# Kernel optimization log

Hardware: AMD Instinct MI355X
Metric: run time of the kernel (lower is better)

## Reference

```python
import jax, jax.numpy as jnp
import numpy as np

BATCH = 32      # init batch_size
HID = 256       # init hidden_dim
SENT = 64       # sentence_size
WORDS = 64      # words per sentence (the -1 in the view)
N = BATCH * SENT


def setup_inputs() -> dict:
    key = jax.random.key(0)
    k1, k2, k3, k4 = jax.random.split(key, 4)
    stdv_lin = 1.0 / np.sqrt(HID)
    x = jax.random.normal(k1, (N, WORDS, HID), dtype=jnp.float32)
    W = jax.random.uniform(k2, (HID, HID), jnp.float32, -stdv_lin, stdv_lin)
    b = jax.random.uniform(k3, (HID,), jnp.float32, -stdv_lin, stdv_lin)
    context = jax.random.uniform(k4, (HID,), jnp.float32, -stdv_lin, stdv_lin)
    return {"x": x, "W": W, "b": b, "context": context, "sentence_size": SENT}


def reference(x, W, b, context, sentence_size):
    # tanh(Linear(x)) applied per position; vectorized over the batch loop
    attends = jnp.tanh(jnp.einsum("nwh,oh->nwo", x, W) + b)  # [N, WORDS, HID]
    scores = attends * context                                 # [N, WORDS, HID]
    # nn.Softmax on the [-1, HID] view -> softmax over the hidden dim
    alpha = jax.nn.softmax(scores, axis=-1)                    # [N, WORDS, HID]
    attended = x * alpha                                       # legacy same-numel mul
    attended = attended.reshape(BATCH, sentence_size, -1, HID)
    return jnp.sum(attended, axis=2)                           # [BATCH, SENT, HID]
```

## Files before the change

kernel.cpp:

```cpp
#include <hip/hip_runtime.h>
#include <hip/hip_bf16.h>

#define HID 256
#define NROWS 2048
#define NITER 8
#define GRID (NROWS / NITER)
#define PITCH 264

typedef __attribute__((ext_vector_type(8))) short short8;
typedef __attribute__((ext_vector_type(4))) float float4v;
typedef __attribute__((ext_vector_type(4))) unsigned short ushort4v;

__device__ __forceinline__ float bf2f(unsigned short u) {
    return __uint_as_float(((unsigned int)u) << 16);
}

__device__ __forceinline__ unsigned int pk_bf16(float a, float b) {
    __hip_bfloat162 p = __float22bfloat162_rn(float2{a, b});
    return *(unsigned int*)&p;
}

__device__ __forceinline__ float tanh_fast(float x) {
    float e = __builtin_amdgcn_exp2f(x * 2.8853900817779268f);
    return 1.0f - 2.0f * __builtin_amdgcn_rcpf(e + 1.0f);
}

__device__ __forceinline__ float exp_small(float s) {
    float p = __builtin_fmaf(s, 0.16666667f, 0.5f);
    p = __builtin_fmaf(p, s, 1.0f);
    return __builtin_fmaf(p, s, 1.0f);
}

__device__ __forceinline__ void barrier_lds_only() {
    __asm__ volatile("" ::: "memory");
    __builtin_amdgcn_s_waitcnt(0xC07F);
    __builtin_amdgcn_s_barrier();
    __asm__ volatile("" ::: "memory");
}

__device__ __forceinline__ float row16_sum(float v) {
    float t;
    t = __builtin_bit_cast(float, __builtin_amdgcn_update_dpp(
            0, __builtin_bit_cast(int, v), 0xB1, 0xf, 0xf, true));
    v += t;
    t = __builtin_bit_cast(float, __builtin_amdgcn_update_dpp(
            0, __builtin_bit_cast(int, v), 0x4E, 0xf, 0xf, true));
    v += t;
    t = __builtin_bit_cast(float, __builtin_amdgcn_update_dpp(
            0, __builtin_bit_cast(int, v), 0x124, 0xf, 0xf, true));
    v += t;
    t = __builtin_bit_cast(float, __builtin_amdgcn_update_dpp(
            0, __builtin_bit_cast(int, v), 0x128, 0xf, 0xf, true));
    v += t;
    return v;
}

__global__ void cvt_w(const float* __restrict__ W, unsigned short* __restrict__ Wb) {
    int i = blockIdx.x * 256 + threadIdx.x;
    float4v v = ((const float4v*)W)[i];
    unsigned int lo = pk_bf16(v.x, v.y), hi = pk_bf16(v.z, v.w);
    ushort4v u;
    u.x = (unsigned short)lo; u.y = (unsigned short)(lo >> 16);
    u.z = (unsigned short)hi; u.w = (unsigned short)(hi >> 16);
    ((ushort4v*)Wb)[i] = u;
}

__global__ __launch_bounds__(512, 2) void attend_fused(
    const float* __restrict__ x, const unsigned short* __restrict__ Wb,
    const float* __restrict__ bias, const float* __restrict__ ctx,
    float* __restrict__ out)
{
    __shared__ unsigned short xs[2][64 * PITCH];
    __shared__ float wsum[8][64];
    __shared__ float rinv[64];

    const int tid  = threadIdx.x;
    const int wave = tid >> 6;
    const int lane = tid & 63;
    const int q    = lane >> 4;
    const int c    = lane & 15;
    const int obase = wave * 32;

    float bb[2], cc[2];
#pragma unroll
    for (int nt = 0; nt < 2; ++nt) {
        bb[nt] = bias[obase + 2 * c + nt];
        cc[nt] = ctx[obase + 2 * c + nt];
    }
    short8 bfrag[8][2];
#pragma unroll
    for (int nt = 0; nt < 2; ++nt) {
        const unsigned short* wr = &Wb[(size_t)(obase + 2 * c + nt) * 256 + q * 8];
#pragma unroll
        for (int kt = 0; kt < 8; ++kt)
            bfrag[kt][nt] = *(const short8*)(wr + kt * 32);
    }

    const int n0 = blockIdx.x * NITER;

    {
        const float4v* xg = (const float4v*)(x + (size_t)n0 * (64 * 256));
        float4v v0[8];
#pragma unroll
        for (int i = 0; i < 8; ++i)
            v0[i] = xg[tid + 512 * i];
#pragma unroll
        for (int i = 0; i < 8; ++i) {
            const int chunk = tid + 512 * i;
            const int r = chunk >> 6, col4 = (chunk & 63) * 4;
            uint2 u;
            u.x = pk_bf16(v0[i].x, v0[i].y);
            u.y = pk_bf16(v0[i].z, v0[i].w);
            *(uint2*)&xs[0][r * PITCH + col4] = u;
        }
    }
    __syncthreads();

    for (int it = 0; it < NITER; ++it) {
        const int n = n0 + it;
        const int cur = it & 1;

        float4v vbuf[8];
        if (it + 1 < NITER) {
            const float4v* xg = (const float4v*)(x + (size_t)(n + 1) * (64 * 256));
#pragma unroll
            for (int i = 0; i < 8; ++i)
                vbuf[i] = xg[tid + 512 * i];
        }

        float4v acc[4][2];
#pragma unroll
        for (int mt = 0; mt < 4; ++mt)
#pragma unroll
            for (int nt = 0; nt < 2; ++nt)
                acc[mt][nt] = (float4v){0.f, 0.f, 0.f, 0.f};

#pragma unroll
        for (int kt = 0; kt < 8; ++kt) {
            short8 a[4];
#pragma unroll
            for (int mt = 0; mt < 4; ++mt)
                a[mt] = *(const short8*)&xs[cur][(mt * 16 + c) * PITCH + kt * 32 + q * 8];
#pragma unroll
            for (int nt = 0; nt < 2; ++nt)
#pragma unroll
                for (int mt = 0; mt < 4; ++mt)
                    acc[mt][nt] = __builtin_amdgcn_mfma_f32_16x16x32_bf16(
                        a[mt], bfrag[kt][nt], acc[mt][nt], 0, 0, 0);
        }

        float psum[4][4];
#pragma unroll
        for (int mt = 0; mt < 4; ++mt)
#pragma unroll
            for (int r = 0; r < 4; ++r)
                psum[mt][r] = 0.f;

#pragma unroll
        for (int nt = 0; nt < 2; ++nt) {
#pragma unroll
            for (int mt = 0; mt < 4; ++mt) {
#pragma unroll
                for (int r = 0; r < 4; ++r) {
                    float s = tanh_fast(acc[mt][nt][r] + bb[nt]) * cc[nt];
                    float e = exp_small(s);
                    acc[mt][nt][r] = e;
                    psum[mt][r] += e;
                }
            }
        }
#pragma unroll
        for (int mt = 0; mt < 4; ++mt)
#pragma unroll
            for (int r = 0; r < 4; ++r)
                psum[mt][r] = row16_sum(psum[mt][r]);
        if (c == 0) {
#pragma unroll
            for (int mt = 0; mt < 4; ++mt)
#pragma unroll
                for (int r = 0; r < 4; ++r)
                    wsum[wave][mt * 16 + q * 4 + r] = psum[mt][r];
        }
        barrier_lds_only();
        if (tid < 64) {
            float t = wsum[0][tid] + wsum[1][tid] + wsum[2][tid] + wsum[3][tid]
                    + wsum[4][tid] + wsum[5][tid] + wsum[6][tid] + wsum[7][tid];
            rinv[tid] = __builtin_amdgcn_rcpf(t);
        }
        barrier_lds_only();

        float ri[4][4];
#pragma unroll
        for (int mt = 0; mt < 4; ++mt)
#pragma unroll
            for (int r = 0; r < 4; ++r)
                ri[mt][r] = rinv[mt * 16 + q * 4 + r];

        float outp[2] = {0.f, 0.f};
#pragma unroll
        for (int mt = 0; mt < 4; ++mt) {
#pragma unroll
            for (int r = 0; r < 4; ++r) {
                const int w = mt * 16 + q * 4 + r;
                unsigned int pair = *(const unsigned int*)&xs[cur][w * PITCH + obase + 2 * c];
                const float wgt = ri[mt][r];
                outp[0] += bf2f((unsigned short)pair)         * (acc[mt][0][r] * wgt);
                outp[1] += bf2f((unsigned short)(pair >> 16)) * (acc[mt][1][r] * wgt);
            }
        }
#pragma unroll
        for (int nt = 0; nt < 2; ++nt) {
            float v = outp[nt];
            v += __shfl_xor(v, 16);
            v += __shfl_xor(v, 32);
            outp[nt] = v;
        }
        if (q == 0)
            *(float2*)&out[(size_t)n * HID + obase + 2 * c] = float2{outp[0], outp[1]};

        if (it + 1 < NITER) {
#pragma unroll
            for (int i = 0; i < 8; ++i) {
                const int chunk = tid + 512 * i;
                const int r = chunk >> 6, col4 = (chunk & 63) * 4;
                uint2 u;
                u.x = pk_bf16(vbuf[i].x, vbuf[i].y);
                u.y = pk_bf16(vbuf[i].z, vbuf[i].w);
                *(uint2*)&xs[cur ^ 1][r * PITCH + col4] = u;
            }
            __syncthreads();
        }
    }
}

extern "C" void kernel_launch(void* const* d_in, const int* in_sizes, int n_in,
                              void* d_out, int out_size, void* d_ws, size_t ws_size,
                              hipStream_t stream) {
    const float* x    = (const float*)d_in[0];
    const float* W    = (const float*)d_in[1];
    const float* bias = (const float*)d_in[2];
    const float* ctx  = (const float*)d_in[3];
    unsigned short* Wb = (unsigned short*)d_ws;

    cvt_w<<<64, 256, 0, stream>>>(W, Wb);
    attend_fused<<<GRID, 512, 0, stream>>>(x, Wb, bias, ctx, (float*)d_out);
}
```

Baseline: 207.7 us.

## Use 256-thread blocks with 64 columns per wave and stream W fragments

Halves the block size to 4 waves, each computing 64 output columns instead of 32, and halves rows per block so the grid doubles. Instead of keeping all W bf16 fragments resident in registers, each k-step reloads W from global/L2 with a one-step-ahead prefetch, freeing registers for the larger accumulator tile and the 16-deep x prefetch buffer. The intent is more blocks and better latency hiding with fewer waves in the softmax reduction. The cost is repeated W loads from cache in every iteration and a larger per-thread x staging buffer.

Measured after the change: 265.6 us. 27.9% more time.

```diff
diff --git a/kernel.cpp b/kernel.cpp
--- a/kernel.cpp
+++ b/kernel.cpp
@@ -3,7 +3,7 @@
 
 #define HID 256
 #define NROWS 2048
-#define NITER 8
+#define NITER 4
 #define GRID (NROWS / NITER)
 #define PITCH 264
 
@@ -65,13 +65,13 @@
     ((ushort4v*)Wb)[i] = u;
 }
 
-__global__ __launch_bounds__(512, 2) void attend_fused(
+__global__ __launch_bounds__(256, 2) void attend_fused(
     const float* __restrict__ x, const unsigned short* __restrict__ Wb,
     const float* __restrict__ bias, const float* __restrict__ ctx,
     float* __restrict__ out)
 {
     __shared__ unsigned short xs[2][64 * PITCH];
-    __shared__ float wsum[8][64];
+    __shared__ float wsum[4][64];
     __shared__ float rinv[64];
 
     const int tid  = threadIdx.x;
@@ -79,34 +79,35 @@
     const int lane = tid & 63;
     const int q    = lane >> 4;
     const int c    = lane & 15;
-    const int obase = wave * 32;
-
-    float bb[2], cc[2];
-#pragma unroll
-    for (int nt = 0; nt < 2; ++nt) {
-        bb[nt] = bias[obase + 2 * c + nt];
-        cc[nt] = ctx[obase + 2 * c + nt];
+    const int obase = wave * 64;
+
+    int col[4];
+#pragma unroll
+    for (int nt = 0; nt < 4; ++nt)
+        col[nt] = obase + (nt >> 1) * 32 + 2 * c + (nt & 1);
+
+    float bb[4], cc[4];
+#pragma unroll
+    for (int nt = 0; nt < 4; ++nt) {
+        bb[nt] = bias[col[nt]];
+        cc[nt] = ctx[col[nt]];
     }
-    short8 bfrag[8][2];
-#pragma unroll
-    for (int nt = 0; nt < 2; ++nt) {
-        const unsigned short* wr = &Wb[(size_t)(obase + 2 * c + nt) * 256 + q * 8];
-#pragma unroll
-        for (int kt = 0; kt < 8; ++kt)
-            bfrag[kt][nt] = *(const short8*)(wr + kt * 32);
-    }
+    const unsigned short* wrow[4];
+#pragma unroll
+    for (int nt = 0; nt < 4; ++nt)
+        wrow[nt] = &Wb[(size_t)col[nt] * 256 + q * 8];
 
     const int n0 = blockIdx.x * NITER;
 
     {
         const float4v* xg = (const float4v*)(x + (size_t)n0 * (64 * 256));
-        float4v v0[8];
-#pragma unroll
-        for (int i = 0; i < 8; ++i)
-            v0[i] = xg[tid + 512 * i];
-#pragma unroll
-        for (int i = 0; i < 8; ++i) {
-            const int chunk = tid + 512 * i;
+        float4v v0[16];
+#pragma unroll
+        for (int i = 0; i < 16; ++i)
+            v0[i] = xg[tid + 256 * i];
+#pragma unroll
+        for (int i = 0; i < 16; ++i) {
+            const int chunk = tid + 256 * i;
             const int r = chunk >> 6, col4 = (chunk & 63) * 4;
             uint2 u;
             u.x = pk_bf16(v0[i].x, v0[i].y);
@@ -120,33 +121,46 @@
         const int n = n0 + it;
         const int cur = it & 1;
 
-        float4v vbuf[8];
+        float4v vbuf[16];
         if (it + 1 < NITER) {
             const float4v* xg = (const float4v*)(x + (size_t)(n + 1) * (64 * 256));
 #pragma unroll
-            for (int i = 0; i < 8; ++i)
-                vbuf[i] = xg[tid + 512 * i];
-        }
-
-        float4v acc[4][2];
-#pragma unroll
-        for (int mt = 0; mt < 4; ++mt)
-#pragma unroll
-            for (int nt = 0; nt < 2; ++nt)
+            for (int i = 0; i < 16; ++i)
+                vbuf[i] = xg[tid + 256 * i];
+        }
+
+        float4v acc[4][4];
+#pragma unroll
+        for (int mt = 0; mt < 4; ++mt)
+#pragma unroll
+            for (int nt = 0; nt < 4; ++nt)
                 acc[mt][nt] = (float4v){0.f, 0.f, 0.f, 0.f};
 
+        short8 bcur[4], bnxt[4];
+#pragma unroll
+        for (int nt = 0; nt < 4; ++nt)
+            bcur[nt] = *(const short8*)(wrow[nt]);
+
 #pragma unroll
         for (int kt = 0; kt < 8; ++kt) {
+            if (kt < 7) {
+#pragma unroll
+                for (int nt = 0; nt < 4; ++nt)
+                    bnxt[nt] = *(const short8*)(wrow[nt] + (kt + 1) * 32);
+            }
             short8 a[4];
 #pragma unroll
             for (int mt = 0; mt < 4; ++mt)
                 a[mt] = *(const short8*)&xs[cur][(mt * 16 + c) * PITCH + kt * 32 + q * 8];
 #pragma unroll
-            for (int nt = 0; nt < 2; ++nt)
+            for (int nt = 0; nt < 4; ++nt)
 #pragma unroll
                 for (int mt = 0; mt < 4; ++mt)
                     acc[mt][nt] = __builtin_amdgcn_mfma_f32_16x16x32_bf16(
-                        a[mt], bfrag[kt][nt], acc[mt][nt], 0, 0, 0);
+                        a[mt], bcur[nt], acc[mt][nt], 0, 0, 0);
+#pragma unroll
+            for (int nt = 0; nt < 4; ++nt)
+                bcur[nt] = bnxt[nt];
         }
 
         float psum[4][4];
@@ -157,7 +171,7 @@
                 psum[mt][r] = 0.f;
 
 #pragma unroll
-        for (int nt = 0; nt < 2; ++nt) {
+        for (int nt = 0; nt < 4; ++nt) {
 #pragma unroll
             for (int mt = 0; mt < 4; ++mt) {
 #pragma unroll
@@ -183,8 +197,7 @@
         }
         barrier_lds_only();
         if (tid < 64) {
-            float t = wsum[0][tid] + wsum[1][tid] + wsum[2][tid] + wsum[3][tid]
-                    + wsum[4][tid] + wsum[5][tid] + wsum[6][tid] + wsum[7][tid];
+            float t = wsum[0][tid] + wsum[1][tid] + wsum[2][tid] + wsum[3][tid];
             rinv[tid] = __builtin_amdgcn_rcpf(t);
         }
         barrier_lds_only();
@@ -196,32 +209,37 @@
             for (int r = 0; r < 4; ++r)
                 ri[mt][r] = rinv[mt * 16 + q * 4 + r];
 
-        float outp[2] = {0.f, 0.f};
+        float outp[4] = {0.f, 0.f, 0.f, 0.f};
 #pragma unroll
         for (int mt = 0; mt < 4; ++mt) {
 #pragma unroll
             for (int r = 0; r < 4; ++r) {
                 const int w = mt * 16 + q * 4 + r;
-                unsigned int pair = *(const unsigned int*)&xs[cur][w * PITCH + obase + 2 * c];
                 const float wgt = ri[mt][r];
-                outp[0] += bf2f((unsigned short)pair)         * (acc[mt][0][r] * wgt);
-                outp[1] += bf2f((unsigned short)(pair >> 16)) * (acc[mt][1][r] * wgt);
-            }
-        }
-#pragma unroll
-        for (int nt = 0; nt < 2; ++nt) {
+                unsigned int p0 = *(const unsigned int*)&xs[cur][w * PITCH + obase + 2 * c];
+                unsigned int p1 = *(const unsigned int*)&xs[cur][w * PITCH + obase + 32 + 2 * c];
+                outp[0] += bf2f((unsigned short)p0)         * (acc[mt][0][r] * wgt);
+                outp[1] += bf2f((unsigned short)(p0 >> 16)) * (acc[mt][1][r] * wgt);
+                outp[2] += bf2f((unsigned short)p1)         * (acc[mt][2][r] * wgt);
+                outp[3] += bf2f((unsigned short)(p1 >> 16)) * (acc[mt][3][r] * wgt);
+            }
+        }
+#pragma unroll
+        for (int nt = 0; nt < 4; ++nt) {
             float v = outp[nt];
             v += __shfl_xor(v, 16);
             v += __shfl_xor(v, 32);
             outp[nt] = v;
         }
-        if (q == 0)
-            *(float2*)&out[(size_t)n * HID + obase + 2 * c] = float2{outp[0], outp[1]};
+        if (q == 0) {
+            *(float2*)&out[(size_t)n * HID + obase + 2 * c]      = float2{outp[0], outp[1]};
+            *(float2*)&out[(size_t)n * HID + obase + 32 + 2 * c] = float2{outp[2], outp[3]};
+        }
 
         if (it + 1 < NITER) {
 #pragma unroll
-            for (int i = 0; i < 8; ++i) {
-                const int chunk = tid + 512 * i;
+            for (int i = 0; i < 16; ++i) {
+                const int chunk = tid + 256 * i;
                 const int r = chunk >> 6, col4 = (chunk & 63) * 4;
                 uint2 u;
                 u.x = pk_bf16(vbuf[i].x, vbuf[i].y);
@@ -243,5 +261,5 @@
     unsigned short* Wb = (unsigned short*)d_ws;
 
     cvt_w<<<64, 256, 0, stream>>>(W, Wb);
-    attend_fused<<<GRID, 512, 0, stream>>>(x, Wb, bias, ctx, (float*)d_out);
-}
+    attend_fused<<<GRID, 256, 0, stream>>>(x, Wb, bias, ctx, (float*)d_out);
+}
```
